# Kernel optimization log

Hardware: AMD Instinct MI355X
Metric: run time of the kernel (lower is better)

The kernel has to match this reference:

```python
import jax, jax.numpy as jnp
import numpy as np
import math

NUM_HEADS = 12
POS_BND = 16                 # patch_num
RPE_NUM = 2 * POS_BND + 1    # 33
LOGIT_SCALE_MAX = math.log(1.0 / 0.01)
EPS_NORM = 1e-12


def setup_inputs() -> dict:
    key = jax.random.key(0)
    ks = jax.random.split(key, 8)
    L, N, C = 257, 32, 768   # L = 16*16 patches + 1 CLS
    H, W = 16, 16
    x = jax.random.normal(ks[0], (L, N, C), dtype=jnp.float32)
    depth = jax.random.uniform(ks[1], (N, 1, H, W), dtype=jnp.float32)
    in_proj_w = jax.random.normal(ks[2], (3 * C, C), dtype=jnp.float32) * 0.02
    in_proj_b = jnp.zeros((3 * C,), dtype=jnp.float32)
    out_proj_w = jax.random.normal(ks[3], (C, C), dtype=jnp.float32) * 0.02
    out_proj_b = jnp.zeros((C,), dtype=jnp.float32)
    rpe_table = jax.random.normal(ks[4], (3 * RPE_NUM, NUM_HEADS), dtype=jnp.float32) * 0.02
    logit_scale = jnp.log(10.0) * jnp.ones((NUM_HEADS, 1, 1), dtype=jnp.float32)
    return {
        "x": x, "depth": depth,
        "in_proj_w": in_proj_w, "in_proj_b": in_proj_b,
        "out_proj_w": out_proj_w, "out_proj_b": out_proj_b,
        "rpe_table": rpe_table, "logit_scale": logit_scale,
    }


def _rpe_bias(depth, rpe_table):
    # depth: (B, 1, H, W) -> bias (B*num_heads, H*W, H*W)
    d = depth[:, 0]                              # (B, H, W)
    B, H, W = d.shape
    ii, jj = jnp.meshgrid(jnp.arange(H), jnp.arange(W), indexing="ij")
    xg = (jj.astype(jnp.float32) / (W - 1))[None].repeat(B, axis=0)   # (B,H,W)
    yg = (ii.astype(jnp.float32) / (H - 1))[None].repeat(B, axis=0)
    z_min = d.min(axis=(-2, -1), keepdims=True)
    z_max = d.max(axis=(-2, -1), keepdims=True)
    z = (d - z_min) / (z_max - z_min + 1e-8)
    coords = jnp.stack([xg, yg, z], axis=-1).reshape(B, H * W, 3)     # (B,HW,3)
    rel = coords[:, :, None, :] - coords[:, None, :, :]               # (B,HW,HW,3)
    idx = jnp.clip(jnp.round(rel * POS_BND).astype(jnp.int32), -POS_BND, POS_BND)
    idx = idx + POS_BND + jnp.arange(3, dtype=jnp.int32) * RPE_NUM    # (B,HW,HW,3)
    bias = rpe_table[idx].sum(axis=3)                                 # (B,HW,HW,heads)
    bias = bias.transpose(0, 3, 1, 2)                                 # (B,heads,HW,HW)
    return bias.reshape(-1, H * W, H * W)


def reference(x, depth, in_proj_w, in_proj_b, out_proj_w, out_proj_b, rpe_table, logit_scale):
    L, N, C = x.shape
    Hn = NUM_HEADS
    hd = C // Hn
    qkv = x @ in_proj_w.T + in_proj_b                     # (L,N,3C)
    q, k, v = jnp.split(qkv, 3, axis=-1)
    def to_heads(t):
        return t.reshape(L, N * Hn, hd).transpose(1, 0, 2)  # (N*Hn, L, hd)
    q, k, v = to_heads(q), to_heads(k), to_heads(v)
    # scaled-cosine attention: normalized q,k then clamped exp(log-scale)
    qn = q / jnp.maximum(jnp.linalg.norm(q, axis=-1, keepdims=True), EPS_NORM)
    kn = k / jnp.maximum(jnp.linalg.norm(k, axis=-1, keepdims=True), EPS_NORM)
    attn = jnp.einsum("bld,bmd->blm", qn, kn)             # (N*Hn, L, L)
    scale = jnp.exp(jnp.minimum(logit_scale, LOGIT_SCALE_MAX))   # (Hn,1,1)
    attn = (attn.reshape(N, Hn, L, L) * scale).reshape(N * Hn, L, L)
    # relative-position bias on patch tokens (skip CLS at index 0)
    res = _rpe_bias(depth, rpe_table)                     # (N*Hn, L-1, L-1)
    attn = attn.at[:, 1:, 1:].add(res)
    attn = jax.nn.softmax(attn, axis=-1)
    out = jnp.einsum("blm,bmd->bld", attn, v)             # (N*Hn, L, hd)
    out = out.transpose(1, 0, 2).reshape(L, N, C)
    out = out @ out_proj_w.T + out_proj_b
    return out, attn
```

## Files before the change

kernel.cpp:

```cpp
#include <hip/hip_runtime.h>
#include <math.h>

#define L_TOK 257
#define N_B 32
#define C_DIM 768
#define N_H 12
#define HD 64
#define BH (N_B * N_H)
#define M_TOK (L_TOK * N_B)
#define HW 256
#define RPE_NUM 33
#define LOGIT_MAX 4.6051701859880913680f
#define VT_STRIDE 264
#define MT_Q 65
#define NT_Q 18
#define NT_O 12

typedef unsigned short ushort;
typedef unsigned int uint;
typedef __attribute__((ext_vector_type(8))) short short8;
typedef __attribute__((ext_vector_type(4))) float f32x4;

__device__ __forceinline__ ushort f2bf_rn(float f) {
  uint u = __float_as_uint(f);
  uint r = (u + 0x7FFF + ((u >> 16) & 1)) >> 16;
  return (ushort)r;
}
__device__ __forceinline__ float bf2f(ushort h) {
  return __uint_as_float(((uint)h) << 16);
}

__device__ __forceinline__ int xcd_swz(int wid, int nwg) {
  int q = nwg >> 3, r = nwg & 7;
  int xcd = wid & 7, pos = wid >> 3;
  int base = (xcd < r) ? xcd * (q + 1) : r * (q + 1) + (xcd - r) * q;
  return base + pos;
}

__device__ __forceinline__ void tile_map(int bid, int MT, int NT, int nwg,
                                         int& m0, int& nt) {
  int wid = xcd_swz(bid, nwg);
  int per = 8 * NT;
  int s = wid / per;
  int rem = wid - s * per;
  int msz = MT - s * 8; if (msz > 8) msz = 8;
  int mi = rem % msz, ni = rem / msz;
  m0 = (s * 8 + mi) * 128;
  nt = ni;
}

__global__ __launch_bounds__(256)
void cvt_split(const float* __restrict__ src, ushort* __restrict__ hi,
               ushort* __restrict__ lo, int n) {
  int i = (blockIdx.x * 256 + threadIdx.x) * 4;
  if (i + 3 >= n + 3) return;
  if (i + 3 < n) {
    float4 v = *(const float4*)(src + i);
    ushort h0 = f2bf_rn(v.x), h1 = f2bf_rn(v.y), h2 = f2bf_rn(v.z), h3 = f2bf_rn(v.w);
    ushort l0 = f2bf_rn(v.x - bf2f(h0)), l1 = f2bf_rn(v.y - bf2f(h1));
    ushort l2 = f2bf_rn(v.z - bf2f(h2)), l3 = f2bf_rn(v.w - bf2f(h3));
    *(ushort4*)(hi + i) = make_ushort4(h0, h1, h2, h3);
    *(ushort4*)(lo + i) = make_ushort4(l0, l1, l2, l3);
  } else {
    for (int k = i; k < n; ++k) {
      float vv = src[k];
      ushort h = f2bf_rn(vv);
      hi[k] = h; lo[k] = f2bf_rn(vv - bf2f(h));
    }
  }
}

__global__ __launch_bounds__(256)
void gemm_out_n64(const ushort* __restrict__ Ahi, const ushort* __restrict__ Alo,
                  const ushort* __restrict__ Bhi, const ushort* __restrict__ Blo,
                  const float* __restrict__ bias, float* __restrict__ Cout) {
  __shared__ __align__(16) ushort lds[12288];
  ushort* sAh = lds;
  ushort* sAl = lds + 4096;
  ushort* sBh = lds + 8192;
  ushort* sBl = lds + 10240;

  const int M = M_TOK, Nn = C_DIM, K = C_DIM;
  const int t = threadIdx.x;
  const int wave = t >> 6, lane = t & 63;
  const int wm = (wave & 1) * 64;
  const int wn = (wave >> 1) * 32;
  int m0, nt;
  tile_map(blockIdx.x, MT_Q, NT_O, MT_Q * NT_O, m0, nt);
  const int n0 = nt * 64;

  const int ar = t >> 2;
  const int ac = (t & 3) * 8;
  const uint ldsOff = (uint)(t & 192) * 16;

  const int frm = lane & 15;
  const int frk = (lane >> 4) * 8;

  f32x4 acc[4][2] = {};

  for (int k0 = 0; k0 < K; k0 += 32) {
#pragma unroll
    for (int half = 0; half < 2; ++half) {
      int rA = m0 + half * 64 + ar; if (rA > M - 1) rA = M - 1;
      size_t gA = (size_t)rA * K + k0 + ac;
      uint so = (uint)half * 4096 + ldsOff;
      __builtin_amdgcn_global_load_lds(
          (const __attribute__((address_space(1))) void*)(Ahi + gA),
          (__attribute__((address_space(3))) void*)((char*)sAh + so), 16, 0, 0);
      __builtin_amdgcn_global_load_lds(
          (const __attribute__((address_space(1))) void*)(Alo + gA),
          (__attribute__((address_space(3))) void*)((char*)sAl + so), 16, 0, 0);
    }
    {
      int rB = n0 + ar;
      size_t gB = (size_t)rB * K + k0 + ac;
      __builtin_amdgcn_global_load_lds(
          (const __attribute__((address_space(1))) void*)(Bhi + gB),
          (__attribute__((address_space(3))) void*)((char*)sBh + ldsOff), 16, 0, 0);
      __builtin_amdgcn_global_load_lds(
          (const __attribute__((address_space(1))) void*)(Blo + gB),
          (__attribute__((address_space(3))) void*)((char*)sBl + ldsOff), 16, 0, 0);
    }
    __syncthreads();

    short8 ah[4], al[4], bh[2], bl[2];
#pragma unroll
    for (int i = 0; i < 4; ++i) {
      int r = wm + i * 16 + frm;
      ah[i] = *(const short8*)(sAh + r * 32 + frk);
      al[i] = *(const short8*)(sAl + r * 32 + frk);
    }
#pragma unroll
    for (int j = 0; j < 2; ++j) {
      int c = wn + j * 16 + frm;
      bh[j] = *(const short8*)(sBh + c * 32 + frk);
      bl[j] = *(const short8*)(sBl + c * 32 + frk);
    }
#pragma unroll
    for (int i = 0; i < 4; ++i)
#pragma unroll
      for (int j = 0; j < 2; ++j) {
        acc[i][j] = __builtin_amdgcn_mfma_f32_16x16x32_bf16(ah[i], bh[j], acc[i][j], 0, 0, 0);
        acc[i][j] = __builtin_amdgcn_mfma_f32_16x16x32_bf16(ah[i], bl[j], acc[i][j], 0, 0, 0);
        acc[i][j] = __builtin_amdgcn_mfma_f32_16x16x32_bf16(al[i], bh[j], acc[i][j], 0, 0, 0);
      }
    __syncthreads();
  }

  const int ecol = lane & 15;
#pragma unroll
  for (int j = 0; j < 2; ++j) {
    int col = n0 + wn + j * 16 + ecol;
    float bv = bias[col];
#pragma unroll
    for (int i = 0; i < 4; ++i) {
      int rbase = m0 + wm + i * 16 + (lane >> 4) * 4;
#pragma unroll
      for (int r = 0; r < 4; ++r) {
        int row = rbase + r;
        if (row < M) Cout[(size_t)row * Nn + col] = acc[i][j][r] + bv;
      }
    }
  }
}

__global__ __launch_bounds__(256)
void gemm_qkv_fused(const ushort* __restrict__ Ahi, const ushort* __restrict__ Alo,
                    const ushort* __restrict__ Bhi, const ushort* __restrict__ Blo,
                    const float* __restrict__ bias,
                    ushort* __restrict__ qhi, ushort* __restrict__ qlo,
                    ushort* __restrict__ khi, ushort* __restrict__ klo,
                    float* __restrict__ vout) {
  __shared__ __align__(16) ushort lds[4 * 128 * 32];
  ushort* sAh = lds;
  ushort* sAl = lds + 4096;
  ushort* sBh = lds + 8192;
  ushort* sBl = lds + 12288;

  const int K = C_DIM, M = M_TOK;
  const int t = threadIdx.x;
  const int wave = t >> 6, lane = t & 63;
  const int wm = (wave & 1) * 64;
  const int wn = (wave >> 1) * 64;
  int m0, nt;
  tile_map(blockIdx.x, MT_Q, NT_Q, MT_Q * NT_Q, m0, nt);
  const int n0 = nt * 128;

  const int ar = t >> 2;
  const int ac = (t & 3) * 8;
  const uint ldsOff = (uint)(t & 192) * 16;

  const int frm = lane & 15;
  const int frk = (lane >> 4) * 8;

  f32x4 acc[4][4] = {};

  for (int k0 = 0; k0 < K; k0 += 32) {
#pragma unroll
    for (int half = 0; half < 2; ++half) {
      int rA = m0 + half * 64 + ar; if (rA > M - 1) rA = M - 1;
      int rB = n0 + half * 64 + ar;
      size_t gA = (size_t)rA * K + k0 + ac;
      size_t gB = (size_t)rB * K + k0 + ac;
      uint so = (uint)half * 4096 + ldsOff;
      __builtin_amdgcn_global_load_lds(
          (const __attribute__((address_space(1))) void*)(Ahi + gA),
          (__attribute__((address_space(3))) void*)((char*)sAh + so), 16, 0, 0);
      __builtin_amdgcn_global_load_lds(
          (const __attribute__((address_space(1))) void*)(Alo + gA),
          (__attribute__((address_space(3))) void*)((char*)sAl + so), 16, 0, 0);
      __builtin_amdgcn_global_load_lds(
          (const __attribute__((address_space(1))) void*)(Bhi + gB),
          (__attribute__((address_space(3))) void*)((char*)sBh + so), 16, 0, 0);
      __builtin_amdgcn_global_load_lds(
          (const __attribute__((address_space(1))) void*)(Blo + gB),
          (__attribute__((address_space(3))) void*)((char*)sBl + so), 16, 0, 0);
    }
    __syncthreads();

    short8 ah[4], al[4], bh[4], bl[4];
#pragma unroll
    for (int i = 0; i < 4; ++i) {
      int r = wm + i * 16 + frm;
      ah[i] = *(const short8*)(sAh + r * 32 + frk);
      al[i] = *(const short8*)(sAl + r * 32 + frk);
      int c = wn + i * 16 + frm;
      bh[i] = *(const short8*)(sBh + c * 32 + frk);
      bl[i] = *(const short8*)(sBl + c * 32 + frk);
    }
#pragma unroll
    for (int i = 0; i < 4; ++i)
#pragma unroll
      for (int j = 0; j < 4; ++j) {
        acc[i][j] = __builtin_amdgcn_mfma_f32_16x16x32_bf16(ah[i], bh[j], acc[i][j], 0, 0, 0);
        acc[i][j] = __builtin_amdgcn_mfma_f32_16x16x32_bf16(ah[i], bl[j], acc[i][j], 0, 0, 0);
        acc[i][j] = __builtin_amdgcn_mfma_f32_16x16x32_bf16(al[i], bh[j], acc[i][j], 0, 0, 0);
      }
    __syncthreads();
  }

  const int c0 = lane & 15, g = lane >> 4;
  const int colBase = n0 + wn;
  const int sect = colBase / C_DIM;
  const int hh = (colBase - sect * C_DIM) >> 6;
  float bv[4];
#pragma unroll
  for (int j = 0; j < 4; ++j) bv[j] = bias[colBase + j * 16 + c0];

#pragma unroll
  for (int i = 0; i < 4; ++i) {
#pragma unroll
    for (int r = 0; r < 4; ++r) {
      const int row = m0 + wm + i * 16 + g * 4 + r;
      float lv[4];
#pragma unroll
      for (int j = 0; j < 4; ++j) lv[j] = acc[i][j][r] + bv[j];
      if (sect == 2) {
        if (row < M) {
          int l = row >> 5, n = row & 31;
          size_t ob = ((size_t)((n * N_H + hh) * L_TOK + l)) * HD;
#pragma unroll
          for (int j = 0; j < 4; ++j) vout[ob + j * 16 + c0] = lv[j];
        }
      } else {
        float ss = lv[0] * lv[0] + lv[1] * lv[1] + lv[2] * lv[2] + lv[3] * lv[3];
        ss += __shfl_xor(ss, 1);
        ss += __shfl_xor(ss, 2);
        ss += __shfl_xor(ss, 4);
        ss += __shfl_xor(ss, 8);
        float inv = 1.0f / fmaxf(sqrtf(ss), 1e-12f);
        if (row < M) {
          int l = row >> 5, n = row & 31;
          size_t ob = ((size_t)((n * N_H + hh) * L_TOK + l)) * HD;
          ushort* dh = sect ? khi : qhi;
          ushort* dl = sect ? klo : qlo;
#pragma unroll
          for (int j = 0; j < 4; ++j) {
            float val = lv[j] * inv;
            ushort hv = f2bf_rn(val);
            dh[ob + j * 16 + c0] = hv;
            dl[ob + j * 16 + c0] = f2bf_rn(val - bf2f(hv));
          }
        }
      }
    }
  }
}

__global__ __launch_bounds__(256)
void vt_make(const float* __restrict__ v, ushort* __restrict__ vthi,
             ushort* __restrict__ vtlo) {
  __shared__ float sT[64][65];
  const int b = blockIdx.x;
  const int t = threadIdx.x;
  const float* vb = v + (size_t)b * L_TOK * HD;
  ushort* vh = vthi + (size_t)b * HD * VT_STRIDE;
  ushort* vl = vtlo + (size_t)b * HD * VT_STRIDE;
  for (int k0 = 0; k0 < 256; k0 += 64) {
#pragma unroll
    for (int p = 0; p < 16; ++p) {
      int idx = p * 256 + t;
      int k = idx >> 6, d = idx & 63;
      sT[d][k] = vb[(size_t)(k0 + k) * HD + d];
    }
    __syncthreads();
#pragma unroll
    for (int p = 0; p < 16; ++p) {
      int idx = p * 256 + t;
      int d = idx >> 6, k = idx & 63;
      float val = sT[d][k];
      ushort h = f2bf_rn(val);
      vh[(size_t)d * VT_STRIDE + k0 + k] = h;
      vl[(size_t)d * VT_STRIDE + k0 + k] = f2bf_rn(val - bf2f(h));
    }
    __syncthreads();
  }
  if (t < HD) {
    float val = vb[(size_t)256 * HD + t];
    ushort h = f2bf_rn(val);
    vh[(size_t)t * VT_STRIDE + 256] = h;
    vl[(size_t)t * VT_STRIDE + 256] = f2bf_rn(val - bf2f(h));
  }
}

__global__ __launch_bounds__(256)
void attn_mfma(const ushort* __restrict__ qhi, const ushort* __restrict__ qlo,
               const ushort* __restrict__ khi, const ushort* __restrict__ klo,
               const float* __restrict__ depth, const float* __restrict__ rpe,
               const float* __restrict__ lscale, float* __restrict__ P) {
  __shared__ __align__(16) ushort sKh[256 * 72];
  __shared__ __align__(16) ushort sKl[256 * 72];
  __shared__ float cz_s[HW];
  __shared__ float txd[32], tyd[32], tzt[36];
  __shared__ float red_s[16];
  __shared__ float s256[4][16];

  const int tile = blockIdx.x;
  const int b = blockIdx.y;
  const int n = b / N_H, h = b - n * N_H;
  const int t = threadIdx.x;
  const int lane = t & 63, wave = t >> 6;

  float dval = depth[n * HW + t];
  float mn = dval, mx = dval;
#pragma unroll
  for (int o = 32; o > 0; o >>= 1) {
    mn = fminf(mn, __shfl_down(mn, o));
    mx = fmaxf(mx, __shfl_down(mx, o));
  }
  if (lane == 0) { red_s[wave] = mn; red_s[8 + wave] = mx; }
  __syncthreads();
  float zmin = fminf(fminf(red_s[0], red_s[1]), fminf(red_s[2], red_s[3]));
  float zmax = fmaxf(fmaxf(red_s[8], red_s[9]), fmaxf(red_s[10], red_s[11]));
  float den = zmax - zmin + 1e-8f;
  cz_s[t] = (dval - zmin) / den;
  if (t < 31) {
    int d = t - 15;
    int ix = (int)rintf((float)d * (16.0f / 15.0f));
    ix = max(-16, min(16, ix));
    txd[t] = rpe[(ix + 16) * N_H + h];
    tyd[t] = rpe[(RPE_NUM + ix + 16) * N_H + h];
  }
  if (t < RPE_NUM) tzt[t] = rpe[(2 * RPE_NUM + t) * N_H + h];
  const float scale = expf(fminf(lscale[h], LOGIT_MAX));

  const ushort* khb = khi + (size_t)b * L_TOK * HD;
  const ushort* klb = klo + (size_t)b * L_TOK * HD;
#pragma unroll
  for (int it = 0; it < 8; ++it) {
    int idx = it * 256 + t;
    int j = idx >> 3, c = (idx & 7) * 8;
    *(uint4*)(sKh + j * 72 + c) = *(const uint4*)(khb + (size_t)j * HD + c);
    *(uint4*)(sKl + j * 72 + c) = *(const uint4*)(klb + (size_t)j * HD + c);
  }
  __syncthreads();

  const int qrow = tile * 64 + 16 * wave;
  const size_t qoff = ((size_t)b * L_TOK + qrow + (lane & 15)) * HD + (lane >> 4) * 8;
  short8 qh0 = *(const short8*)(qhi + qoff);
  short8 qh1 = *(const short8*)(qhi + qoff + 32);
  short8 ql0 = *(const short8*)(qlo + qoff);
  short8 ql1 = *(const short8*)(qlo + qoff + 32);

  f32x4 acc[16] = {};
#pragma unroll
  for (int jt = 0; jt < 16; ++jt) {
    const ushort* bp = sKh + (jt * 16 + (lane & 15)) * 72 + (lane >> 4) * 8;
    const ushort* bq = sKl + (jt * 16 + (lane & 15)) * 72 + (lane >> 4) * 8;
    short8 bh0 = *(const short8*)(bp);
    short8 bh1 = *(const short8*)(bp + 32);
    short8 bl0 = *(const short8*)(bq);
    short8 bl1 = *(const short8*)(bq + 32);
    acc[jt] = __builtin_amdgcn_mfma_f32_16x16x32_bf16(qh0, bh0, acc[jt], 0, 0, 0);
    acc[jt] = __builtin_amdgcn_mfma_f32_16x16x32_bf16(qh1, bh1, acc[jt], 0, 0, 0);
    acc[jt] = __builtin_amdgcn_mfma_f32_16x16x32_bf16(qh0, bl0, acc[jt], 0, 0, 0);
    acc[jt] = __builtin_amdgcn_mfma_f32_16x16x32_bf16(qh1, bl1, acc[jt], 0, 0, 0);
    acc[jt] = __builtin_amdgcn_mfma_f32_16x16x32_bf16(ql0, bh0, acc[jt], 0, 0, 0);
    acc[jt] = __builtin_amdgcn_mfma_f32_16x16x32_bf16(ql1, bh1, acc[jt], 0, 0, 0);
  }

  {
    const ushort* k6h = khb + (size_t)256 * HD + (lane >> 4) * 8;
    const ushort* k6l = klb + (size_t)256 * HD + (lane >> 4) * 8;
    float p = 0.f;
#pragma unroll
    for (int j = 0; j < 8; ++j) {
      float kf0 = bf2f(k6h[j]) + bf2f(k6l[j]);
      float kf1 = bf2f(k6h[32 + j]) + bf2f(k6l[32 + j]);
      float qf0 = bf2f((ushort)qh0[j]) + bf2f((ushort)ql0[j]);
      float qf1 = bf2f((ushort)qh1[j]) + bf2f((ushort)ql1[j]);
      p = fmaf(qf0, kf0, fmaf(qf1, kf1, p));
    }
    p += __shfl_xor(p, 16);
    p += __shfl_xor(p, 32);
    if (lane < 16) s256[wave][lane] = p;
  }

  const int g = lane >> 4, c0 = lane & 15;

  float lg6[4];
#pragma unroll
  for (int r = 0; r < 4; ++r) {
    int gi = tile * 64 + 16 * wave + 4 * g + r;
    float d6 = s256[wave][4 * g + r];
    float bz = 0.f;
    if (gi >= 1) {
      int dx = ((gi - 1) & 15) - 15;
      int dy = ((gi - 1) >> 4) - 15;
      float rz = (cz_s[gi - 1] - cz_s[255]) * 16.0f;
      int iz = (int)rintf(rz); iz = max(-16, min(16, iz));
      bz = txd[dx + 15] + tyd[dy + 15] + tzt[iz + 16];
    }
    lg6[r] = scale * d6 + bz;
  }

#pragma unroll
  for (int jt = 0; jt < 16; ++jt) {
    int col = jt * 16 + c0;
#pragma unroll
    for (int r = 0; r < 4; ++r) {
      int gi = tile * 64 + 16 * wave + 4 * g + r;
      float lv = scale * acc[jt][r];
      if (col >= 1 && gi >= 1) {
        int dx = ((gi - 1) & 15) - ((col - 1) & 15);
        int dy = ((gi - 1) >> 4) - ((col - 1) >> 4);
        float rz = (cz_s[gi - 1] - cz_s[col - 1]) * 16.0f;
        int iz = (int)rintf(rz); iz = max(-16, min(16, iz));
        lv += txd[dx + 15] + tyd[dy + 15] + tzt[iz + 16];
      }
      acc[jt][r] = lv;
    }
  }

  float* Pb_ = P + (size_t)b * L_TOK * L_TOK;
#pragma unroll
  for (int r = 0; r < 4; ++r) {
    int gi = tile * 64 + 16 * wave + 4 * g + r;
    float m = acc[0][r];
#pragma unroll
    for (int jt = 1; jt < 16; ++jt) m = fmaxf(m, acc[jt][r]);
#pragma unroll
    for (int o = 1; o < 16; o <<= 1) m = fmaxf(m, __shfl_xor(m, o));
    m = fmaxf(m, lg6[r]);
    float s = 0.f;
#pragma unroll
    for (int jt = 0; jt < 16; ++jt) {
      float e = __expf(acc[jt][r] - m);
      acc[jt][r] = e;
      s += e;
    }
#pragma unroll
    for (int o = 1; o < 16; o <<= 1) s += __shfl_xor(s, o);
    float e6 = __expf(lg6[r] - m);
    float inv = 1.0f / (s + e6);
    float* Prow = Pb_ + (size_t)gi * L_TOK;
#pragma unroll
    for (int jt = 0; jt < 16; ++jt)
      Prow[jt * 16 + c0] = acc[jt][r] * inv;
    if (c0 == 0) Prow[256] = e6 * inv;
  }
}

__global__ __launch_bounds__(256)
void attn_row256(const ushort* __restrict__ qhi, const ushort* __restrict__ qlo,
                 const ushort* __restrict__ khi, const ushort* __restrict__ klo,
                 const float* __restrict__ depth, const float* __restrict__ rpe,
                 const float* __restrict__ lscale, float* __restrict__ P) {
  __shared__ float qs[HD];
  __shared__ float cz_s[HW];
  __shared__ float txd[32], tyd[32], tzt[36];
  __shared__ float red_s[16];
  __shared__ float lg6_sh;

  const int b = blockIdx.x;
  const int n = b / N_H, h = b - n * N_H;
  const int t = threadIdx.x;
  const int lane = t & 63, wave = t >> 6;

  float dval = depth[n * HW + t];
  float mn = dval, mx = dval;
#pragma unroll
  for (int o = 32; o > 0; o >>= 1) {
    mn = fminf(mn, __shfl_down(mn, o));
    mx = fmaxf(mx, __shfl_down(mx, o));
  }
  if (lane == 0) { red_s[wave] = mn; red_s[8 + wave] = mx; }
  __syncthreads();
  float zmin = fminf(fminf(red_s[0], red_s[1]), fminf(red_s[2], red_s[3]));
  float zmax = fmaxf(fmaxf(red_s[8], red_s[9]), fmaxf(red_s[10], red_s[11]));
  float den = zmax - zmin + 1e-8f;
  cz_s[t] = (dval - zmin) / den;
  if (t < 31) {
    int d = t - 15;
    int ix = (int)rintf((float)d * (16.0f / 15.0f));
    ix = max(-16, min(16, ix));
    txd[t] = rpe[(ix + 16) * N_H + h];
    tyd[t] = rpe[(RPE_NUM + ix + 16) * N_H + h];
  }
  if (t < RPE_NUM) tzt[t] = rpe[(2 * RPE_NUM + t) * N_H + h];
  const float scale = expf(fminf(lscale[h], LOGIT_MAX));

  const size_t q6 = ((size_t)b * L_TOK + 256) * HD;
  if (t < HD) qs[t] = bf2f(qhi[q6 + t]) + bf2f(qlo[q6 + t]);
  __syncthreads();

  const ushort* krh = khi + ((size_t)b * L_TOK + t) * HD;
  const ushort* krl = klo + ((size_t)b * L_TOK + t) * HD;
  float dot = 0.f;
#pragma unroll
  for (int c = 0; c < HD; c += 8) {
    ushort4 hv0 = *(const ushort4*)(krh + c);
    ushort4 hv1 = *(const ushort4*)(krh + c + 4);
    ushort4 lv0 = *(const ushort4*)(krl + c);
    ushort4 lv1 = *(const ushort4*)(krl + c + 4);
    dot = fmaf(bf2f(hv0.x) + bf2f(lv0.x), qs[c + 0], dot);
    dot = fmaf(bf2f(hv0.y) + bf2f(lv0.y), qs[c + 1], dot);
    dot = fmaf(bf2f(hv0.z) + bf2f(lv0.z), qs[c + 2], dot);
    dot = fmaf(bf2f(hv0.w) + bf2f(lv0.w), qs[c + 3], dot);
    dot = fmaf(bf2f(hv1.x) + bf2f(lv1.x), qs[c + 4], dot);
    dot = fmaf(bf2f(hv1.y) + bf2f(lv1.y), qs[c + 5], dot);
    dot = fmaf(bf2f(hv1.z) + bf2f(lv1.z), qs[c + 6], dot);
    dot = fmaf(bf2f(hv1.w) + bf2f(lv1.w), qs[c + 7], dot);
  }

  float lg;
  {
    float bsum = 0.f;
    if (t >= 1) {
      int dx = 15 - ((t - 1) & 15);
      int dy = 15 - ((t - 1) >> 4);
      float rz = (cz_s[255] - cz_s[t - 1]) * 16.0f;
      int iz = (int)rintf(rz); iz = max(-16, min(16, iz));
      bsum = txd[dx + 15] + tyd[dy + 15] + tzt[iz + 16];
    }
    lg = scale * dot + bsum;
  }

  if (wave == 0) {
    const ushort* k6h = khi + q6;
    const ushort* k6l = klo + q6;
    float pp = (bf2f(k6h[lane]) + bf2f(k6l[lane])) * qs[lane];
#pragma unroll
    for (int o = 32; o > 0; o >>= 1) pp += __shfl_down(pp, o);
    if (lane == 0) {
      float bz = txd[15] + tyd[15] + tzt[16];
      lg6_sh = scale * pp + bz;
    }
  }

  float m = lg;
#pragma unroll
  for (int o = 32; o > 0; o >>= 1) m = fmaxf(m, __shfl_down(m, o));
  if (lane == 0) red_s[wave] = m;
  __syncthreads();
  float M = fmaxf(fmaxf(red_s[0], red_s[1]), fmaxf(red_s[2], red_s[3]));
  M = fmaxf(M, lg6_sh);
  float e = __expf(lg - M);
  float s = e;
#pragma unroll
  for (int o = 32; o > 0; o >>= 1) s += __shfl_down(s, o);
  if (lane == 0) red_s[8 + wave] = s;
  __syncthreads();
  float e6 = __expf(lg6_sh - M);
  float S = (red_s[8] + red_s[9]) + (red_s[10] + red_s[11]) + e6;
  float inv = 1.0f / S;
  float* Prow = P + (size_t)b * L_TOK * L_TOK + (size_t)256 * L_TOK;
  Prow[t] = e * inv;
  if (t == 0) Prow[256] = e6 * inv;
}

__global__ __launch_bounds__(256)
void pv_mfma(const float* __restrict__ P, const ushort* __restrict__ vthi,
             const ushort* __restrict__ vtlo, const float* __restrict__ v,
             ushort* __restrict__ ahi, ushort* __restrict__ alo) {
  const int b = blockIdx.y;
  const int n = b / N_H, h = b - n * N_H;
  const int t = threadIdx.x;
  const int lane = t & 63, wave = t >> 6;
  const int rbase = blockIdx.x * 128 + wave * 32;
  const float* Pb = P + (size_t)b * L_TOK * L_TOK;
  const ushort* vh = vthi + (size_t)b * HD * VT_STRIDE;
  const ushort* vl = vtlo + (size_t)b * HD * VT_STRIDE;

  const int fm = lane & 15, fk = (lane >> 4) * 8;
  f32x4 acc[2][4] = {};

  for (int k0 = 0; k0 < 256; k0 += 32) {
    short8 ah[2], al[2], bh[4], bl[4];
#pragma unroll
    for (int i = 0; i < 2; ++i) {
      const float* pr = Pb + (size_t)(rbase + i * 16 + fm) * L_TOK + k0 + fk;
#pragma unroll
      for (int j = 0; j < 8; ++j) {
        float pv_ = pr[j];
        ushort hh = f2bf_rn(pv_);
        ah[i][j] = (short)hh;
        al[i][j] = (short)f2bf_rn(pv_ - bf2f(hh));
      }
    }
#pragma unroll
    for (int j = 0; j < 4; ++j) {
      const ushort* bp = vh + (size_t)(j * 16 + fm) * VT_STRIDE + k0 + fk;
      const ushort* bq = vl + (size_t)(j * 16 + fm) * VT_STRIDE + k0 + fk;
      bh[j] = *(const short8*)bp;
      bl[j] = *(const short8*)bq;
    }
#pragma unroll
    for (int i = 0; i < 2; ++i)
#pragma unroll
      for (int j = 0; j < 4; ++j) {
        acc[i][j] = __builtin_amdgcn_mfma_f32_16x16x32_bf16(ah[i], bh[j], acc[i][j], 0, 0, 0);
        acc[i][j] = __builtin_amdgcn_mfma_f32_16x16x32_bf16(ah[i], bl[j], acc[i][j], 0, 0, 0);
        acc[i][j] = __builtin_amdgcn_mfma_f32_16x16x32_bf16(al[i], bh[j], acc[i][j], 0, 0, 0);
        acc[i][j] = __builtin_amdgcn_mfma_f32_16x16x32_bf16(al[i], bl[j], acc[i][j], 0, 0, 0);
      }
  }

  const int g = lane >> 4;
  float v6[4];
#pragma unroll
  for (int j = 0; j < 4; ++j)
    v6[j] = v[((size_t)b * L_TOK + 256) * HD + j * 16 + fm];
#pragma unroll
  for (int i = 0; i < 2; ++i)
#pragma unroll
    for (int r = 0; r < 4; ++r) {
      int row = rbase + i * 16 + g * 4 + r;
      float p6 = Pb[(size_t)row * L_TOK + 256];
#pragma unroll
      for (int j = 0; j < 4; ++j) acc[i][j][r] += p6 * v6[j];
    }

#pragma unroll
  for (int i = 0; i < 2; ++i)
#pragma unroll
    for (int r = 0; r < 4; ++r) {
      int row = rbase + i * 16 + g * 4 + r;
      size_t o = ((size_t)row * N_B + n) * C_DIM + h * HD;
#pragma unroll
      for (int j = 0; j < 4; ++j) {
        float val = acc[i][j][r];
        ushort hv = f2bf_rn(val);
        ahi[o + j * 16 + fm] = hv;
        alo[o + j * 16 + fm] = f2bf_rn(val - bf2f(hv));
      }
    }

  if (blockIdx.x == 0 && t < HD) {
    const float* Prow = Pb + (size_t)256 * L_TOK;
    const float* vb = v + (size_t)b * L_TOK * HD;
    float sum = 0.f;
    for (int k = 0; k < L_TOK; ++k)
      sum = fmaf(Prow[k], vb[(size_t)k * HD + t], sum);
    size_t o = ((size_t)256 * N_B + n) * C_DIM + h * HD + t;
    ushort hv = f2bf_rn(sum);
    ahi[o] = hv;
    alo[o] = f2bf_rn(sum - bf2f(hv));
  }
}

extern "C" void kernel_launch(void* const* d_in, const int* in_sizes, int n_in,
                              void* d_out, int out_size, void* d_ws, size_t ws_size,
                              hipStream_t stream) {
  const float* x      = (const float*)d_in[0];
  const float* depth  = (const float*)d_in[1];
  const float* w_in   = (const float*)d_in[2];
  const float* b_in   = (const float*)d_in[3];
  const float* w_out  = (const float*)d_in[4];
  const float* b_out  = (const float*)d_in[5];
  const float* rpe    = (const float*)d_in[6];
  const float* lscale = (const float*)d_in[7];
  float* out = (float*)d_out;
  float* ws = (float*)d_ws;

  ushort* xhi  = (ushort*)ws;
  ushort* xlo  = xhi + 6316032;
  ushort* vthi = (ushort*)(ws + 6316032);
  ushort* vtlo = vthi + 6488064;
  float*  v    = ws + 18948096;
  ushort* qhi  = (ushort*)(ws + 25264128);
  ushort* qlo  = qhi + 6316032;
  ushort* khi  = qlo + 6316032;
  ushort* klo  = khi + 6316032;
  ushort* wihi = (ushort*)(ws + 37896192);
  ushort* wilo = wihi + 1769472;
  ushort* wohi = wilo + 1769472;
  ushort* wolo = wohi + 589824;
  ushort* ahi  = xhi;
  ushort* alo  = xlo;
  float* Pout = out + 6316032;

  cvt_split<<<6168, 256, 0, stream>>>(x, xhi, xlo, 6316032);
  cvt_split<<<1728, 256, 0, stream>>>(w_in, wihi, wilo, 1769472);
  cvt_split<<<576, 256, 0, stream>>>(w_out, wohi, wolo, 589824);

  gemm_qkv_fused<<<MT_Q * NT_Q, 256, 0, stream>>>(xhi, xlo, wihi, wilo, b_in,
                                                  qhi, qlo, khi, klo, v);
  vt_make<<<BH, 256, 0, stream>>>(v, vthi, vtlo);
  attn_mfma<<<dim3(4, BH), 256, 0, stream>>>(qhi, qlo, khi, klo, depth, rpe, lscale, Pout);
  attn_row256<<<BH, 256, 0, stream>>>(qhi, qlo, khi, klo, depth, rpe, lscale, Pout);
  pv_mfma<<<dim3(2, BH), 256, 0, stream>>>(Pout, vthi, vtlo, v, ahi, alo);

  gemm_out_n64<<<MT_Q * NT_O, 256, 0, stream>>>(ahi, alo, wohi, wolo, b_out, out);
}
```

Measured before the change: 494.1 us.

## Pipeline split-bf16 GEMMs with double-buffered LDS, swizzle, and phased waits

Both projection GEMMs now share a common core that double-buffers the LDS tiles. It issues the next k-tile's global-to-LDS loads while computing the current one, and splits each k-step into three MFMA phases (hi*hi, lo*hi, hi*lo) with fine-grained vmcnt waits and s_setprio around MFMA bursts. LDS rows are XOR-swizzled to cut bank conflicts. The output GEMM moves from 64-wide to 128-wide N tiles, which gives it more reuse but half as many blocks. LDS use doubles to 64KB, which may reduce occupancy, and the hand-placed waitcnt counts must stay exactly matched to the load order.

```diff
diff --git a/kernel.cpp b/kernel.cpp
--- a/kernel.cpp
+++ b/kernel.cpp
@@ -14,7 +14,8 @@
 #define VT_STRIDE 264
 #define MT_Q 65
 #define NT_Q 18
-#define NT_O 12
+#define NT_O 6
+#define NTK 24
 
 typedef unsigned short ushort;
 typedef unsigned int uint;
@@ -70,97 +71,142 @@
   }
 }
 
-__global__ __launch_bounds__(256)
-void gemm_out_n64(const ushort* __restrict__ Ahi, const ushort* __restrict__ Alo,
-                  const ushort* __restrict__ Bhi, const ushort* __restrict__ Blo,
-                  const float* __restrict__ bias, float* __restrict__ Cout) {
-  __shared__ __align__(16) ushort lds[12288];
-  ushort* sAh = lds;
-  ushort* sAl = lds + 4096;
-  ushort* sBh = lds + 8192;
-  ushort* sBl = lds + 10240;
-
-  const int M = M_TOK, Nn = C_DIM, K = C_DIM;
+__device__ __forceinline__ void stage_pair(const ushort* g0, const ushort* g1,
+                                           ushort* l, uint so) {
+  __builtin_amdgcn_global_load_lds(
+      (const __attribute__((address_space(1))) void*)g0,
+      (__attribute__((address_space(3))) void*)((char*)l + so), 16, 0, 0);
+  __builtin_amdgcn_global_load_lds(
+      (const __attribute__((address_space(1))) void*)g1,
+      (__attribute__((address_space(3))) void*)((char*)l + so + 4096), 16, 0, 0);
+}
+
+#define PH_WAIT(N)                                        \
+  asm volatile("s_waitcnt vmcnt(" #N ")" ::: "memory");   \
+  __builtin_amdgcn_s_barrier();                           \
+  __builtin_amdgcn_sched_barrier(0);
+
+#define PH_LGKM()                                         \
+  asm volatile("s_waitcnt lgkmcnt(0)" ::: "memory");      \
+  __builtin_amdgcn_sched_barrier(0);
+
+__device__ __forceinline__ void gemm3_core(
+    const ushort* __restrict__ Ahi, const ushort* __restrict__ Alo,
+    const ushort* __restrict__ Bhi, const ushort* __restrict__ Blo,
+    int m0, int n0, ushort* lds, f32x4 (&acc)[4][4]) {
+  const int K = C_DIM, M = M_TOK;
   const int t = threadIdx.x;
   const int wave = t >> 6, lane = t & 63;
-  const int wm = (wave & 1) * 64;
-  const int wn = (wave >> 1) * 32;
-  int m0, nt;
-  tile_map(blockIdx.x, MT_Q, NT_O, MT_Q * NT_O, m0, nt);
-  const int n0 = nt * 64;
+  const int wm = (wave & 1) * 64, wn = (wave >> 1) * 64;
+  const int frm = lane & 15, fs = lane >> 4;
+  const int sx = (fs ^ ((frm >> 1) & 3)) * 8;
 
   const int ar = t >> 2;
-  const int ac = (t & 3) * 8;
-  const uint ldsOff = (uint)(t & 192) * 16;
-
-  const int frm = lane & 15;
-  const int frk = (lane >> 4) * 8;
-
-  f32x4 acc[4][2] = {};
-
-  for (int k0 = 0; k0 < K; k0 += 32) {
-#pragma unroll
-    for (int half = 0; half < 2; ++half) {
-      int rA = m0 + half * 64 + ar; if (rA > M - 1) rA = M - 1;
-      size_t gA = (size_t)rA * K + k0 + ac;
-      uint so = (uint)half * 4096 + ldsOff;
-      __builtin_amdgcn_global_load_lds(
-          (const __attribute__((address_space(1))) void*)(Ahi + gA),
-          (__attribute__((address_space(3))) void*)((char*)sAh + so), 16, 0, 0);
-      __builtin_amdgcn_global_load_lds(
-          (const __attribute__((address_space(1))) void*)(Alo + gA),
-          (__attribute__((address_space(3))) void*)((char*)sAl + so), 16, 0, 0);
-    }
-    {
-      int rB = n0 + ar;
-      size_t gB = (size_t)rB * K + k0 + ac;
-      __builtin_amdgcn_global_load_lds(
-          (const __attribute__((address_space(1))) void*)(Bhi + gB),
-          (__attribute__((address_space(3))) void*)((char*)sBh + ldsOff), 16, 0, 0);
-      __builtin_amdgcn_global_load_lds(
-          (const __attribute__((address_space(1))) void*)(Blo + gB),
-          (__attribute__((address_space(3))) void*)((char*)sBl + ldsOff), 16, 0, 0);
-    }
-    __syncthreads();
-
-    short8 ah[4], al[4], bh[2], bl[2];
+  const int acs = ((t & 3) ^ ((ar >> 1) & 3)) * 8;
+  const uint so = (uint)(t & 192) * 16;
+
+  int rA0 = m0 + ar;      if (rA0 > M - 1) rA0 = M - 1;
+  int rA1 = m0 + 64 + ar; if (rA1 > M - 1) rA1 = M - 1;
+  const size_t gA0 = (size_t)rA0 * K + acs;
+  const size_t gA1 = (size_t)rA1 * K + acs;
+  const size_t gB0 = (size_t)(n0 + ar) * K + acs;
+  const size_t gB1 = (size_t)(n0 + 64 + ar) * K + acs;
+
+  stage_pair(Ahi + gA0, Ahi + gA1, lds, so);
+  stage_pair(Bhi + gB0, Bhi + gB1, lds + 4096, so);
+  stage_pair(Alo + gA0, Alo + gA1, lds + 8192, so);
+  stage_pair(Blo + gB0, Blo + gB1, lds + 12288, so);
+
+  short8 ah[4], bh[4], al[4], bl[4];
+
+#pragma unroll 2
+  for (int kt = 0; kt < NTK - 1; ++kt) {
+    const int curo = (kt & 1) << 14;
+    const int nxo = curo ^ 16384;
+    const int kn = (kt + 1) * 32;
+    PH_WAIT(4)
 #pragma unroll
     for (int i = 0; i < 4; ++i) {
-      int r = wm + i * 16 + frm;
-      ah[i] = *(const short8*)(sAh + r * 32 + frk);
-      al[i] = *(const short8*)(sAl + r * 32 + frk);
-    }
-#pragma unroll
-    for (int j = 0; j < 2; ++j) {
-      int c = wn + j * 16 + frm;
-      bh[j] = *(const short8*)(sBh + c * 32 + frk);
-      bl[j] = *(const short8*)(sBl + c * 32 + frk);
-    }
-#pragma unroll
-    for (int i = 0; i < 4; ++i)
-#pragma unroll
-      for (int j = 0; j < 2; ++j) {
+      ah[i] = *(const short8*)(lds + curo + (wm + i * 16 + frm) * 32 + sx);
+      bh[i] = *(const short8*)(lds + curo + 4096 + (wn + i * 16 + frm) * 32 + sx);
+    }
+    stage_pair(Ahi + gA0 + kn, Ahi + gA1 + kn, lds + nxo, so);
+    stage_pair(Bhi + gB0 + kn, Bhi + gB1 + kn, lds + nxo + 4096, so);
+    PH_LGKM()
+    __builtin_amdgcn_s_setprio(1);
+#pragma unroll
+    for (int i = 0; i < 4; ++i)
+#pragma unroll
+      for (int j = 0; j < 4; ++j)
         acc[i][j] = __builtin_amdgcn_mfma_f32_16x16x32_bf16(ah[i], bh[j], acc[i][j], 0, 0, 0);
+    __builtin_amdgcn_s_setprio(0);
+    __builtin_amdgcn_sched_barrier(0);
+    PH_WAIT(6)
+#pragma unroll
+    for (int i = 0; i < 4; ++i)
+      al[i] = *(const short8*)(lds + curo + 8192 + (wm + i * 16 + frm) * 32 + sx);
+    stage_pair(Alo + gA0 + kn, Alo + gA1 + kn, lds + nxo + 8192, so);
+    PH_LGKM()
+    __builtin_amdgcn_s_setprio(1);
+#pragma unroll
+    for (int i = 0; i < 4; ++i)
+#pragma unroll
+      for (int j = 0; j < 4; ++j)
+        acc[i][j] = __builtin_amdgcn_mfma_f32_16x16x32_bf16(al[i], bh[j], acc[i][j], 0, 0, 0);
+    __builtin_amdgcn_s_setprio(0);
+    __builtin_amdgcn_sched_barrier(0);
+    PH_WAIT(6)
+#pragma unroll
+    for (int i = 0; i < 4; ++i)
+      bl[i] = *(const short8*)(lds + curo + 12288 + (wn + i * 16 + frm) * 32 + sx);
+    stage_pair(Blo + gB0 + kn, Blo + gB1 + kn, lds + nxo + 12288, so);
+    PH_LGKM()
+    __builtin_amdgcn_s_setprio(1);
+#pragma unroll
+    for (int i = 0; i < 4; ++i)
+#pragma unroll
+      for (int j = 0; j < 4; ++j)
         acc[i][j] = __builtin_amdgcn_mfma_f32_16x16x32_bf16(ah[i], bl[j], acc[i][j], 0, 0, 0);
+    __builtin_amdgcn_s_setprio(0);
+    __builtin_amdgcn_sched_barrier(0);
+  }
+  {
+    const int curo = ((NTK - 1) & 1) << 14;
+    PH_WAIT(4)
+#pragma unroll
+    for (int i = 0; i < 4; ++i) {
+      ah[i] = *(const short8*)(lds + curo + (wm + i * 16 + frm) * 32 + sx);
+      bh[i] = *(const short8*)(lds + curo + 4096 + (wn + i * 16 + frm) * 32 + sx);
+    }
+    PH_LGKM()
+#pragma unroll
+    for (int i = 0; i < 4; ++i)
+#pragma unroll
+      for (int j = 0; j < 4; ++j)
+        acc[i][j] = __builtin_amdgcn_mfma_f32_16x16x32_bf16(ah[i], bh[j], acc[i][j], 0, 0, 0);
+    __builtin_amdgcn_sched_barrier(0);
+    PH_WAIT(2)
+#pragma unroll
+    for (int i = 0; i < 4; ++i)
+      al[i] = *(const short8*)(lds + curo + 8192 + (wm + i * 16 + frm) * 32 + sx);
+    PH_LGKM()
+#pragma unroll
+    for (int i = 0; i < 4; ++i)
+#pragma unroll
+      for (int j = 0; j < 4; ++j)
         acc[i][j] = __builtin_amdgcn_mfma_f32_16x16x32_bf16(al[i], bh[j], acc[i][j], 0, 0, 0);
-      }
-    __syncthreads();
-  }
-
-  const int ecol = lane & 15;
-#pragma unroll
-  for (int j = 0; j < 2; ++j) {
-    int col = n0 + wn + j * 16 + ecol;
-    float bv = bias[col];
-#pragma unroll
-    for (int i = 0; i < 4; ++i) {
-      int rbase = m0 + wm + i * 16 + (lane >> 4) * 4;
-#pragma unroll
-      for (int r = 0; r < 4; ++r) {
-        int row = rbase + r;
-        if (row < M) Cout[(size_t)row * Nn + col] = acc[i][j][r] + bv;
-      }
-    }
+    __builtin_amdgcn_sched_barrier(0);
+    PH_WAIT(0)
+#pragma unroll
+    for (int i = 0; i < 4; ++i)
+      bl[i] = *(const short8*)(lds + curo + 12288 + (wn + i * 16 + frm) * 32 + sx);
+    PH_LGKM()
+#pragma unroll
+    for (int i = 0; i < 4; ++i)
+#pragma unroll
+      for (int j = 0; j < 4; ++j)
+        acc[i][j] = __builtin_amdgcn_mfma_f32_16x16x32_bf16(ah[i], bl[j], acc[i][j], 0, 0, 0);
+    __builtin_amdgcn_sched_barrier(0);
   }
 }
 
@@ -171,74 +217,17 @@
                     ushort* __restrict__ qhi, ushort* __restrict__ qlo,
                     ushort* __restrict__ khi, ushort* __restrict__ klo,
                     float* __restrict__ vout) {
-  __shared__ __align__(16) ushort lds[4 * 128 * 32];
-  ushort* sAh = lds;
-  ushort* sAl = lds + 4096;
-  ushort* sBh = lds + 8192;
-  ushort* sBl = lds + 12288;
-
-  const int K = C_DIM, M = M_TOK;
-  const int t = threadIdx.x;
-  const int wave = t >> 6, lane = t & 63;
-  const int wm = (wave & 1) * 64;
-  const int wn = (wave >> 1) * 64;
+  __shared__ __align__(16) ushort lds[32768];
   int m0, nt;
   tile_map(blockIdx.x, MT_Q, NT_Q, MT_Q * NT_Q, m0, nt);
   const int n0 = nt * 128;
-
-  const int ar = t >> 2;
-  const int ac = (t & 3) * 8;
-  const uint ldsOff = (uint)(t & 192) * 16;
-
-  const int frm = lane & 15;
-  const int frk = (lane >> 4) * 8;
-
   f32x4 acc[4][4] = {};
-
-  for (int k0 = 0; k0 < K; k0 += 32) {
-#pragma unroll
-    for (int half = 0; half < 2; ++half) {
-      int rA = m0 + half * 64 + ar; if (rA > M - 1) rA = M - 1;
-      int rB = n0 + half * 64 + ar;
-      size_t gA = (size_t)rA * K + k0 + ac;
-      size_t gB = (size_t)rB * K + k0 + ac;
-      uint so = (uint)half * 4096 + ldsOff;
-      __builtin_amdgcn_global_load_lds(
-          (const __attribute__((address_space(1))) void*)(Ahi + gA),
-          (__attribute__((address_space(3))) void*)((char*)sAh + so), 16, 0, 0);
-      __builtin_amdgcn_global_load_lds(
-          (const __attribute__((address_space(1))) void*)(Alo + gA),
-          (__attribute__((address_space(3))) void*)((char*)sAl + so), 16, 0, 0);
-      __builtin_amdgcn_global_load_lds(
-          (const __attribute__((address_space(1))) void*)(Bhi + gB),
-          (__attribute__((address_space(3))) void*)((char*)sBh + so), 16, 0, 0);
-      __builtin_amdgcn_global_load_lds(
-          (const __attribute__((address_space(1))) void*)(Blo + gB),
-          (__attribute__((address_space(3))) void*)((char*)sBl + so), 16, 0, 0);
-    }
-    __syncthreads();
-
-    short8 ah[4], al[4], bh[4], bl[4];
-#pragma unroll
-    for (int i = 0; i < 4; ++i) {
-      int r = wm + i * 16 + frm;
-      ah[i] = *(const short8*)(sAh + r * 32 + frk);
-      al[i] = *(const short8*)(sAl + r * 32 + frk);
-      int c = wn + i * 16 + frm;
-      bh[i] = *(const short8*)(sBh + c * 32 + frk);
-      bl[i] = *(const short8*)(sBl + c * 32 + frk);
-    }
-#pragma unroll
-    for (int i = 0; i < 4; ++i)
-#pragma unroll
-      for (int j = 0; j < 4; ++j) {
-        acc[i][j] = __builtin_amdgcn_mfma_f32_16x16x32_bf16(ah[i], bh[j], acc[i][j], 0, 0, 0);
-        acc[i][j] = __builtin_amdgcn_mfma_f32_16x16x32_bf16(ah[i], bl[j], acc[i][j], 0, 0, 0);
-        acc[i][j] = __builtin_amdgcn_mfma_f32_16x16x32_bf16(al[i], bh[j], acc[i][j], 0, 0, 0);
-      }
-    __syncthreads();
-  }
-
+  gemm3_core(Ahi, Alo, Bhi, Blo, m0, n0, lds, acc);
+
+  const int M = M_TOK;
+  const int t = threadIdx.x;
+  const int wave = t >> 6, lane = t & 63;
+  const int wm = (wave & 1) * 64, wn = (wave >> 1) * 64;
   const int c0 = lane & 15, g = lane >> 4;
   const int colBase = n0 + wn;
   const int sect = colBase / C_DIM;
@@ -282,6 +271,38 @@
             dl[ob + j * 16 + c0] = f2bf_rn(val - bf2f(hv));
           }
         }
+      }
+    }
+  }
+}
+
+__global__ __launch_bounds__(256)
+void gemm_out(const ushort* __restrict__ Ahi, const ushort* __restrict__ Alo,
+              const ushort* __restrict__ Bhi, const ushort* __restrict__ Blo,
+              const float* __restrict__ bias, float* __restrict__ Cout) {
+  __shared__ __align__(16) ushort lds[32768];
+  int m0, nt;
+  tile_map(blockIdx.x, MT_Q, NT_O, MT_Q * NT_O, m0, nt);
+  const int n0 = nt * 128;
+  f32x4 acc[4][4] = {};
+  gemm3_core(Ahi, Alo, Bhi, Blo, m0, n0, lds, acc);
+
+  const int M = M_TOK, Nn = C_DIM;
+  const int t = threadIdx.x;
+  const int wave = t >> 6, lane = t & 63;
+  const int wm = (wave & 1) * 64, wn = (wave >> 1) * 64;
+  const int ecol = lane & 15;
+#pragma unroll
+  for (int j = 0; j < 4; ++j) {
+    int col = n0 + wn + j * 16 + ecol;
+    float bv = bias[col];
+#pragma unroll
+    for (int i = 0; i < 4; ++i) {
+      int rbase = m0 + wm + i * 16 + (lane >> 4) * 4;
+#pragma unroll
+      for (int r = 0; r < 4; ++r) {
+        int row = rbase + r;
+        if (row < M) Cout[(size_t)row * Nn + col] = acc[i][j][r] + bv;
       }
     }
   }
@@ -721,5 +742,5 @@
   attn_row256<<<BH, 256, 0, stream>>>(qhi, qlo, khi, klo, depth, rpe, lscale, Pout);
   pv_mfma<<<dim3(2, BH), 256, 0, stream>>>(Pout, vthi, vtlo, v, ahi, alo);
 
-  gemm_out_n64<<<MT_Q * NT_O, 256, 0, stream>>>(ahi, alo, wohi, wolo, b_out, out);
-}
+  gemm_out<<<MT_Q * NT_O, 256, 0, stream>>>(ahi, alo, wohi, wolo, b_out, out);
+}
```

Result: faster. 454.3 us (-8.1%).
